# Kernel tuning notes

Measured on AMD Instinct MI355X. Metric: run time of the kernel, lower is better.

The kernel has to match this reference:

```python
import jax, jax.numpy as jnp
import numpy as np

RGB2GRAY = jnp.array([0.299, 0.587, 0.114], dtype=jnp.float32)

H_IMG, W_IMG = 1080, 1920
NUM, GRID_Y, GRID_X, GRID_W = 1, 16, 16, 8


def _identity_grids(num, grid_y, grid_x, grid_w):
    ident = jnp.array([1., 0, 0, 0, 0, 1., 0, 0, 0, 0, 1., 0], dtype=jnp.float32)
    return jnp.broadcast_to(ident, (num, grid_y, grid_x, grid_w, 12))


def setup_inputs() -> dict:
    key = jax.random.key(0)
    k1, k2 = jax.random.split(key)
    rgb = jax.random.uniform(k1, (3, H_IMG, W_IMG), dtype=jnp.float32)
    # learned grids = identity affine + small perturbation (so slicing is non-trivial)
    grids = _identity_grids(NUM, GRID_Y, GRID_X, GRID_W) \
        + 0.05 * jax.random.normal(k2, (NUM, GRID_Y, GRID_X, GRID_W, 12), dtype=jnp.float32)
    return {"rgb": rgb, "grids": grids, "idx": 0}


def _bilateral_slice(grid, guidance):
    """Trilinear slice. grid: (Hg, Wg, L, 12); guidance: (Hi, Wi) in [0,1].
    Returns (Hi, Wi, 12)."""
    Hg, Wg, L, _ = grid.shape
    Hi, Wi = guidance.shape
    # align_corners-style pixel -> grid coords
    gy = jnp.linspace(0.0, Hg - 1.0, Hi, dtype=jnp.float32)[:, None]   # (Hi,1)
    gx = jnp.linspace(0.0, Wg - 1.0, Wi, dtype=jnp.float32)[None, :]   # (1,Wi)
    gz = jnp.clip(guidance, 0.0, 1.0) * (L - 1.0)                      # (Hi,Wi)

    fy = jnp.floor(gy); wy = gy - fy
    fx = jnp.floor(gx); wx = gx - fx
    fz = jnp.floor(gz); wz = gz - fz
    y0 = jnp.clip(fy.astype(jnp.int32), 0, Hg - 1); y1 = jnp.clip(y0 + 1, 0, Hg - 1)
    x0 = jnp.clip(fx.astype(jnp.int32), 0, Wg - 1); x1 = jnp.clip(x0 + 1, 0, Wg - 1)
    z0 = jnp.clip(fz.astype(jnp.int32), 0, L - 1);  z1 = jnp.clip(z0 + 1, 0, L - 1)

    out = jnp.zeros((Hi, Wi, 12), dtype=grid.dtype)
    for yi, wyi in ((y0, 1.0 - wy), (y1, wy)):
        for xi, wxi in ((x0, 1.0 - wx), (x1, wx)):
            for zi, wzi in ((z0, 1.0 - wz), (z1, wz)):
                w = (wyi * wxi * wzi)[..., None]          # (Hi,Wi,1)
                out = out + grid[yi, xi, zi] * w          # gather -> (Hi,Wi,12)
    return out


def reference(rgb, grids, idx):
    grid = grids[idx]                         # (Hg, Wg, L, 12)
    rgb_hwc = jnp.transpose(rgb, (1, 2, 0))   # (H, W, 3)
    gray = jnp.tensordot(rgb_hwc, RGB2GRAY, axes=([-1], [0]))  # (H, W)
    affine = _bilateral_slice(grid, gray)     # (H, W, 12)
    affine_mat = affine.reshape(-1, 3, 4)     # (H*W, 3, 4)
    rgb_flat = rgb_hwc.reshape(-1, 3)         # (H*W, 3)
    res_rgb = jnp.einsum('nij,nj->ni', affine_mat[..., :3], rgb_flat) + affine_mat[..., 3]
    return (affine_mat, res_rgb)
```

## Files before the change

### kernel.cpp

```cpp
#include <hip/hip_runtime.h>

#define H_IMG 1080
#define W_IMG 1920
#define HW_PIX (H_IMG * W_IMG)
#define GY 16
#define GX 16
#define GL 8
#define CF 12
#define PPB 128
#define TPB (PPB * 3)

__global__ __launch_bounds__(TPB) void bg_kernel(
    const float* __restrict__ rgb,
    const float* __restrict__ grids,
    const int* __restrict__ idxp,
    float* __restrict__ out)
{
    __shared__ float4 sg[72];

    const int tid = threadIdx.x;
    const int y = blockIdx.y;
    const int xbase = blockIdx.x * PPB;

    const float* grid = grids + (size_t)idxp[0] * (GY * GX * GL * CF);

    float gyv = (float)y * (15.0f / 1079.0f);
    float fy = floorf(gyv);
    float wy = gyv - fy;
    int y0 = min(max((int)fy, 0), GY - 1);
    int y1 = min(y0 + 1, GY - 1);

    int xc0 = (int)floorf((float)xbase * (15.0f / 1919.0f));

    if (tid < 72) {
        int xi  = tid / 24;
        int rem = tid - xi * 24;
        int z   = rem / 3;
        int c4  = rem - z * 3;
        int xc  = min(xc0 + xi, GX - 1);
        const float4* c0 = (const float4*)(grid + (size_t)((y0 * GX + xc) * GL + z) * CF) + c4;
        const float4* c1 = (const float4*)(grid + (size_t)((y1 * GX + xc) * GL + z) * CF) + c4;
        float4 a = *c0, b = *c1;
        float wy0 = 1.0f - wy;
        float4 rr;
        rr.x = wy0 * a.x + wy * b.x;
        rr.y = wy0 * a.y + wy * b.y;
        rr.z = wy0 * a.z + wy * b.z;
        rr.w = wy0 * a.w + wy * b.w;
        sg[tid] = rr;
    }
    __syncthreads();

    const int k = tid / 3;
    const int c = tid - k * 3;
    const int x = xbase + k;
    const int p = y * W_IMG + x;

    float r = rgb[p];
    float g = rgb[HW_PIX + p];
    float b = rgb[2 * HW_PIX + p];

    float gray = 0.299f * r + 0.587f * g + 0.114f * b;

    float gxv = (float)x * (15.0f / 1919.0f);
    float fx = floorf(gxv), wx = gxv - fx;
    float gz = fminf(fmaxf(gray, 0.0f), 1.0f) * 7.0f;
    float fz = floorf(gz), wz = gz - fz;

    int x0g = min(max((int)fx, 0), GX - 1);
    int x1g = min(x0g + 1, GX - 1);
    int xi0 = x0g - xc0;
    int xi1 = x1g - xc0;
    int z0 = min(max((int)fz, 0), GL - 1);
    int z1 = min(z0 + 1, GL - 1);

    float w00 = (1.0f - wx) * (1.0f - wz);
    float w01 = (1.0f - wx) * wz;
    float w10 = wx * (1.0f - wz);
    float w11 = wx * wz;

    float4 A = sg[(xi0 * GL + z0) * 3 + c];
    float4 B = sg[(xi0 * GL + z1) * 3 + c];
    float4 C = sg[(xi1 * GL + z0) * 3 + c];
    float4 D = sg[(xi1 * GL + z1) * 3 + c];

    float4 acc;
    acc.x = fmaf(w00, A.x, fmaf(w01, B.x, fmaf(w10, C.x, w11 * D.x)));
    acc.y = fmaf(w00, A.y, fmaf(w01, B.y, fmaf(w10, C.y, w11 * D.y)));
    acc.z = fmaf(w00, A.z, fmaf(w01, B.z, fmaf(w10, C.z, w11 * D.z)));
    acc.w = fmaf(w00, A.w, fmaf(w01, B.w, fmaf(w10, C.w, w11 * D.w)));

    const size_t base3 = (size_t)(y * W_IMG + xbase) * 3;

    ((float4*)out)[base3 + tid] = acc;

    float res = fmaf(acc.x, r, fmaf(acc.y, g, fmaf(acc.z, b, acc.w)));
    out[(size_t)HW_PIX * 12 + base3 + tid] = res;
}

extern "C" void kernel_launch(void* const* d_in, const int* in_sizes, int n_in,
                              void* d_out, int out_size, void* d_ws, size_t ws_size,
                              hipStream_t stream) {
    const float* rgb   = (const float*)d_in[0];
    const float* grids = (const float*)d_in[1];
    const int*   idx   = (const int*)d_in[2];
    float*       out   = (float*)d_out;

    dim3 grid(W_IMG / PPB, H_IMG);
    dim3 block(TPB);
    bg_kernel<<<grid, block, 0, stream>>>(rgb, grids, idx, out);
}
```

Before: 158.4 us.

## Process one image row per block with two pixels per thread

```diff
diff --git a/kernel.cpp b/kernel.cpp
--- a/kernel.cpp
+++ b/kernel.cpp
@@ -7,8 +7,7 @@
 #define GX 16
 #define GL 8
 #define CF 12
-#define PPB 128
-#define TPB (PPB * 3)
+#define TPB 960
 
 __global__ __launch_bounds__(TPB) void bg_kernel(
     const float* __restrict__ rgb,
@@ -16,11 +15,10 @@
     const int* __restrict__ idxp,
     float* __restrict__ out)
 {
-    __shared__ float4 sg[72];
+    __shared__ float4 sg[GX * GL * 3];
 
     const int tid = threadIdx.x;
-    const int y = blockIdx.y;
-    const int xbase = blockIdx.x * PPB;
+    const int y = blockIdx.x;
 
     const float* grid = grids + (size_t)idxp[0] * (GY * GX * GL * CF);
 
@@ -30,14 +28,11 @@
     int y0 = min(max((int)fy, 0), GY - 1);
     int y1 = min(y0 + 1, GY - 1);
 
-    int xc0 = (int)floorf((float)xbase * (15.0f / 1919.0f));
-
-    if (tid < 72) {
-        int xi  = tid / 24;
-        int rem = tid - xi * 24;
+    if (tid < GX * GL * 3) {
+        int xc  = tid / 24;
+        int rem = tid - xc * 24;
         int z   = rem / 3;
         int c4  = rem - z * 3;
-        int xc  = min(xc0 + xi, GX - 1);
         const float4* c0 = (const float4*)(grid + (size_t)((y0 * GX + xc) * GL + z) * CF) + c4;
         const float4* c1 = (const float4*)(grid + (size_t)((y1 * GX + xc) * GL + z) * CF) + c4;
         float4 a = *c0, b = *c1;
@@ -51,51 +46,66 @@
     }
     __syncthreads();
 
-    const int k = tid / 3;
-    const int c = tid - k * 3;
-    const int x = xbase + k;
-    const int p = y * W_IMG + x;
+    const int xp = 2 * tid;
+    const int p = y * W_IMG + xp;
 
-    float r = rgb[p];
-    float g = rgb[HW_PIX + p];
-    float b = rgb[2 * HW_PIX + p];
+    float2 rv = *(const float2*)(rgb + p);
+    float2 gv = *(const float2*)(rgb + HW_PIX + p);
+    float2 bv = *(const float2*)(rgb + 2 * HW_PIX + p);
 
-    float gray = 0.299f * r + 0.587f * g + 0.114f * b;
+    float4 aff[2][3];
+    float  res[2][3];
 
-    float gxv = (float)x * (15.0f / 1919.0f);
-    float fx = floorf(gxv), wx = gxv - fx;
-    float gz = fminf(fmaxf(gray, 0.0f), 1.0f) * 7.0f;
-    float fz = floorf(gz), wz = gz - fz;
+#pragma unroll
+    for (int i = 0; i < 2; ++i) {
+        float r = (i == 0) ? rv.x : rv.y;
+        float g = (i == 0) ? gv.x : gv.y;
+        float b = (i == 0) ? bv.x : bv.y;
 
-    int x0g = min(max((int)fx, 0), GX - 1);
-    int x1g = min(x0g + 1, GX - 1);
-    int xi0 = x0g - xc0;
-    int xi1 = x1g - xc0;
-    int z0 = min(max((int)fz, 0), GL - 1);
-    int z1 = min(z0 + 1, GL - 1);
+        float gray = 0.299f * r + 0.587f * g + 0.114f * b;
 
-    float w00 = (1.0f - wx) * (1.0f - wz);
-    float w01 = (1.0f - wx) * wz;
-    float w10 = wx * (1.0f - wz);
-    float w11 = wx * wz;
+        float gxv = (float)(xp + i) * (15.0f / 1919.0f);
+        float fx = floorf(gxv), wx = gxv - fx;
+        float gz = fminf(fmaxf(gray, 0.0f), 1.0f) * 7.0f;
+        float fz = floorf(gz), wz = gz - fz;
 
-    float4 A = sg[(xi0 * GL + z0) * 3 + c];
-    float4 B = sg[(xi0 * GL + z1) * 3 + c];
-    float4 C = sg[(xi1 * GL + z0) * 3 + c];
-    float4 D = sg[(xi1 * GL + z1) * 3 + c];
+        int x0g = min(max((int)fx, 0), GX - 1);
+        int x1g = min(x0g + 1, GX - 1);
+        int z0 = min(max((int)fz, 0), GL - 1);
+        int z1 = min(z0 + 1, GL - 1);
 
-    float4 acc;
-    acc.x = fmaf(w00, A.x, fmaf(w01, B.x, fmaf(w10, C.x, w11 * D.x)));
-    acc.y = fmaf(w00, A.y, fmaf(w01, B.y, fmaf(w10, C.y, w11 * D.y)));
-    acc.z = fmaf(w00, A.z, fmaf(w01, B.z, fmaf(w10, C.z, w11 * D.z)));
-    acc.w = fmaf(w00, A.w, fmaf(w01, B.w, fmaf(w10, C.w, w11 * D.w)));
+        float w00 = (1.0f - wx) * (1.0f - wz);
+        float w01 = (1.0f - wx) * wz;
+        float w10 = wx * (1.0f - wz);
+        float w11 = wx * wz;
 
-    const size_t base3 = (size_t)(y * W_IMG + xbase) * 3;
+        const float4* A = sg + (x0g * GL + z0) * 3;
+        const float4* B = sg + (x0g * GL + z1) * 3;
+        const float4* C = sg + (x1g * GL + z0) * 3;
+        const float4* D = sg + (x1g * GL + z1) * 3;
 
-    ((float4*)out)[base3 + tid] = acc;
+#pragma unroll
+        for (int j = 0; j < 3; ++j) {
+            float4 va = A[j], vb = B[j], vc = C[j], vd = D[j];
+            float4 o;
+            o.x = fmaf(w00, va.x, fmaf(w01, vb.x, fmaf(w10, vc.x, w11 * vd.x)));
+            o.y = fmaf(w00, va.y, fmaf(w01, vb.y, fmaf(w10, vc.y, w11 * vd.y)));
+            o.z = fmaf(w00, va.z, fmaf(w01, vb.z, fmaf(w10, vc.z, w11 * vd.z)));
+            o.w = fmaf(w00, va.w, fmaf(w01, vb.w, fmaf(w10, vc.w, w11 * vd.w)));
+            aff[i][j] = o;
+        }
+        res[i][0] = fmaf(aff[i][0].x, r, fmaf(aff[i][0].y, g, fmaf(aff[i][0].z, b, aff[i][0].w)));
+        res[i][1] = fmaf(aff[i][1].x, r, fmaf(aff[i][1].y, g, fmaf(aff[i][1].z, b, aff[i][1].w)));
+        res[i][2] = fmaf(aff[i][2].x, r, fmaf(aff[i][2].y, g, fmaf(aff[i][2].z, b, aff[i][2].w)));
+    }
 
-    float res = fmaf(acc.x, r, fmaf(acc.y, g, fmaf(acc.z, b, acc.w)));
-    out[(size_t)HW_PIX * 12 + base3 + tid] = res;
+    float4* ao = (float4*)out + (size_t)p * 3;
+    ao[0] = aff[0][0]; ao[1] = aff[0][1]; ao[2] = aff[0][2];
+    ao[3] = aff[1][0]; ao[4] = aff[1][1]; ao[5] = aff[1][2];
+
+    float* ro = out + (size_t)HW_PIX * 12 + (size_t)p * 3;
+    ro[0] = res[0][0]; ro[1] = res[0][1]; ro[2] = res[0][2];
+    ro[3] = res[1][0]; ro[4] = res[1][1]; ro[5] = res[1][2];
 }
 
 extern "C" void kernel_launch(void* const* d_in, const int* in_sizes, int n_in,
@@ -106,7 +116,7 @@
     const int*   idx   = (const int*)d_in[2];
     float*       out   = (float*)d_out;
 
-    dim3 grid(W_IMG / PPB, H_IMG);
+    dim3 grid(H_IMG);
     dim3 block(TPB);
     bg_kernel<<<grid, block, 0, stream>>>(rgb, grids, idx, out);
 }
```

After: 161.7 us. +2.0%, slower.
